# Kernel optimization log

Measured on AMD Instinct MI355X. Metric: run time of the kernel, lower is better.

## Reference

```python
import jax, jax.numpy as jnp
import numpy as np

B = 64
N_TEXT, N_VIS, N_AC = 256, 32, 32
N = N_TEXT + N_VIS + N_AC  # 320 total graph nodes
HID, HEADS, LAYERS = 512, 8, 2
HEAD_DIM = HID // HEADS
SW_K, SW_P, SF_M, ALPHA, CROSS_P = 6, 0.15, 3, 0.5, 0.3


def build_hybrid_adj():
    """Watts-Strogatz + Barabasi-Albert hybrid adjacency with cross-modal edges (numpy, setup only)."""
    rng = np.random.default_rng(0)
    # small-world ring lattice
    sw = np.zeros((N, N), np.float32)
    idx = np.arange(N)
    for j in range(1, SW_K // 2 + 1):
        sw[idx, (idx + j) % N] = 1.0
        sw[idx, (idx - j) % N] = 1.0
    # rewiring
    for i in range(N):
        for j in range(i + 1, N):
            if sw[i, j] == 1 and rng.random() < SW_P:
                sw[i, j] = sw[j, i] = 0.0
                cand = np.where(sw[i] == 0)[0]
                cand = cand[cand != i]
                if len(cand) > 0:
                    nj = rng.choice(cand)
                    sw[i, nj] = sw[nj, i] = 1.0
    # scale-free (Barabasi-Albert)
    sf = np.zeros((N, N), np.float32)
    for i in range(SF_M + 1):
        for j in range(i + 1, SF_M + 1):
            sf[i, j] = sf[j, i] = 1.0
    deg = sf.sum(1)
    for v in range(SF_M + 1, N):
        prob = deg[:v] / deg[:v].sum()
        targets = rng.choice(v, size=min(SF_M, v), replace=False, p=prob)
        sf[v, targets] = 1.0
        sf[targets, v] = 1.0
        deg = sf.sum(1)
    adj = ((ALPHA * sw + (1.0 - ALPHA) * sf) > 0.3).astype(np.float32)
    # cross-modal edges: text<->visual, text<->acoustic (Bernoulli), visual<->acoustic temporal diagonal
    ts, te = 0, N_TEXT
    vs, ve = te, te + N_VIS
    as_, ae = ve, ve + N_AC
    cm_v = (rng.random((N_TEXT, N_VIS)) < CROSS_P).astype(np.float32)
    adj[ts:te, vs:ve] = np.maximum(adj[ts:te, vs:ve], cm_v)
    adj[vs:ve, ts:te] = adj[ts:te, vs:ve].T
    cm_a = (rng.random((N_TEXT, N_AC)) < CROSS_P).astype(np.float32)
    adj[ts:te, as_:ae] = np.maximum(adj[ts:te, as_:ae], cm_a)
    adj[as_:ae, ts:te] = adj[ts:te, as_:ae].T
    k = min(N_VIS, N_AC)
    adj[vs + np.arange(k), as_ + np.arange(k)] = 1.0
    adj[as_ + np.arange(k), vs + np.arange(k)] = 1.0
    return adj.astype(np.int32)


def setup_inputs() -> dict:
    key = jax.random.key(0)
    ks = jax.random.split(key, 12)
    s = 0.02
    return {
        "text": jax.random.normal(ks[0], (B, N_TEXT, 768), jnp.float32),
        "visual": jax.random.normal(ks[1], (B, N_VIS, 47), jnp.float32),
        "acoustic": jax.random.normal(ks[2], (B, N_AC, 74), jnp.float32),
        "adj": jnp.asarray(build_hybrid_adj()),
        "Wt": jax.random.normal(ks[3], (768, HID), jnp.float32) * s,
        "Wv": jax.random.normal(ks[4], (47, HID), jnp.float32) * s,
        "Wa": jax.random.normal(ks[5], (74, HID), jnp.float32) * s,
        "Wg": jax.random.normal(ks[6], (LAYERS, HEADS, HID, HEAD_DIM), jnp.float32) * s,
        "a_src": jax.random.normal(ks[7], (LAYERS, HEADS, HEAD_DIM), jnp.float32) * s,
        "a_dst": jax.random.normal(ks[8], (LAYERS, HEADS, HEAD_DIM), jnp.float32) * s,
        "edge_logits": jax.random.normal(ks[9], (N, N), jnp.float32) * s,
    }


def _fusion(text, visual, acoustic, adj, Wt, Wv, Wa, Wg, a_src, a_dst, edge_logits):
    # project each modality into shared hidden space and stack as graph nodes
    x = jnp.concatenate([
        jnp.einsum("btd,dh->bth", text, Wt),
        jnp.einsum("bvd,dh->bvh", visual, Wv),
        jnp.einsum("bad,dh->bah", acoustic, Wa),
    ], axis=1)  # [B, N, HID]
    mask = (adj != 0)[None, None, :, :]  # [1,1,N,N]
    for l in range(LAYERS):
        h = jnp.einsum("bnd,hdf->bhnf", x, Wg[l])          # [B,H,N,Fh]
        # a([h_i || h_j]) factorizes: e_ij = a_src.h_i + a_dst.h_j
        fi = jnp.einsum("bhnf,hf->bhn", h, a_src[l])
        fj = jnp.einsum("bhnf,hf->bhn", h, a_dst[l])
        e = jax.nn.leaky_relu(fi[:, :, :, None] + fj[:, :, None, :], 0.2)
        e = e + edge_logits[None, None, :, :]               # learnable topology bias
        e = jnp.where(mask, e, -jnp.inf)                    # adjacency-masked scores
        att = jnp.nan_to_num(jax.nn.softmax(e, axis=-1))    # fully-masked rows -> 0
        out = jnp.einsum("bhij,bhjf->bhif", att, h)         # message passing
        x = out.transpose(0, 2, 1, 3).reshape(x.shape[0], N, HID)  # concat heads
        if l < LAYERS - 1:
            x = jax.nn.elu(x)
    return x  # [B, N, HID] fused node embeddings


def reference(text, visual, acoustic, adj, Wt, Wv, Wa, Wg, a_src, a_dst, edge_logits):
    return _fusion(text, visual, acoustic, adj, Wt, Wv, Wa, Wg, a_src, a_dst, edge_logits)
```

## Files before the change

### kernel.cpp

```cpp
#include <hip/hip_runtime.h>
#include <hip/hip_bf16.h>
#include <math.h>

#define BB 64
#define NN 320
#define NT 256
#define NV 32
#define NA 32
#define HIDD 512
#define NHEAD 8
#define FD 64

typedef __attribute__((ext_vector_type(8))) short bf16x8;
typedef __attribute__((ext_vector_type(4))) float floatx4;

__device__ float me_g[NN * NN];
__device__ float fif_g[512 * NN];
__device__ float fjf_g[512 * NN];
__device__ unsigned short tihi_g[16384 * 768];
__device__ unsigned short tilo_g[16384 * 768];
__device__ unsigned short vihi_g[2048 * 64];
__device__ unsigned short vilo_g[2048 * 64];
__device__ unsigned short achi_g[2048 * 128];
__device__ unsigned short aclo_g[2048 * 128];
__device__ unsigned short xhi_g[20480 * 512];
__device__ unsigned short xlo_g[20480 * 512];
__device__ unsigned short bwhi_g[512 * 768];
__device__ unsigned short bwlo_g[512 * 768];

__device__ __forceinline__ void split1(float v, unsigned short& h, unsigned short& l) {
    unsigned u = __float_as_uint(v);
    unsigned hu = u & 0xFFFF0000u;
    float lf = v - __uint_as_float(hu);
    h = (unsigned short)(hu >> 16);
    l = (unsigned short)(__float_as_uint(lf) >> 16);
}
__device__ __forceinline__ unsigned pack2(unsigned short a, unsigned short b) {
    return (unsigned)a | ((unsigned)b << 16);
}

typedef const __attribute__((address_space(1))) unsigned int* gas1_t;
typedef __attribute__((address_space(3))) unsigned int* las3_t;
__device__ __forceinline__ void gload_lds16(const void* g, void* s) {
    __builtin_amdgcn_global_load_lds((gas1_t)(unsigned long long)g,
                                     (las3_t)(unsigned)(unsigned long long)s,
                                     16, 0, 0);
}

__global__ __launch_bounds__(256) void build_me(
    const int* __restrict__ adj, const float* __restrict__ elog)
{
    const int i4 = (blockIdx.x * 256 + threadIdx.x) * 4;
    const int4   a = *(const int4*)&adj[i4];
    const float4 e = *(const float4*)&elog[i4];
    float4 m;
    m.x = a.x ? __expf(e.x) : 0.f;
    m.y = a.y ? __expf(e.y) : 0.f;
    m.z = a.z ? __expf(e.z) : 0.f;
    m.w = a.w ? __expf(e.w) : 0.f;
    *(float4*)&me_g[i4] = m;
}

__global__ __launch_bounds__(256) void presplit_A(
    const float* __restrict__ src, int M, int K, int nk, int sel)
{
    unsigned short* dh = (sel == 0) ? tihi_g : (sel == 1) ? vihi_g : achi_g;
    unsigned short* dl = (sel == 0) ? tilo_g : (sel == 1) ? vilo_g : aclo_g;
    const unsigned t = blockIdx.x * 256 + threadIdx.x;
    const unsigned lane = t & 63, rec = t >> 6;
    const unsigned kt = rec % (unsigned)nk, g = rec / (unsigned)nk;
    const int row = g * 16 + (lane & 15);
    if (row >= M) return;
    const int k0 = kt * 32 + ((lane >> 4) << 3);
    float v[8];
    if (((K & 3) == 0) && (k0 + 8 <= K)) {
        *(float4*)&v[0] = *(const float4*)&src[(size_t)row * K + k0];
        *(float4*)&v[4] = *(const float4*)&src[(size_t)row * K + k0 + 4];
    } else {
#pragma unroll
        for (int e = 0; e < 8; e++) v[e] = (k0 + e < K) ? src[(size_t)row * K + k0 + e] : 0.f;
    }
    unsigned short h[8], l[8];
#pragma unroll
    for (int e = 0; e < 8; e++) split1(v[e], h[e], l[e]);
    const size_t o = (size_t)t * 8;
    *(uint4*)&dh[o] = make_uint4(pack2(h[0],h[1]), pack2(h[2],h[3]),
                                 pack2(h[4],h[5]), pack2(h[6],h[7]));
    *(uint4*)&dl[o] = make_uint4(pack2(l[0],l[1]), pack2(l[2],l[3]),
                                 pack2(l[4],l[5]), pack2(l[6],l[7]));
}

__global__ __launch_bounds__(64) void presplit_B(
    const float* __restrict__ W, int K, int Kp, int wg_mode)
{
    const int lane = threadIdx.x;
    const int nt = blockIdx.x, kt = blockIdx.y;
    const int col = nt * 16 + (lane & 15);
    const int k0 = kt * 32 + (lane >> 4) * 8;
    unsigned short h[8], l[8];
#pragma unroll
    for (int e = 0; e < 8; e++) {
        const int k = k0 + e;
        float v = 0.f;
        if (k < K) v = wg_mode ? W[(size_t)(col >> 6) * (512 * 64) + (size_t)k * 64 + (col & 63)]
                               : W[(size_t)k * 512 + col];
        split1(v, h[e], l[e]);
    }
    const size_t o = (((size_t)nt * (Kp >> 5) + kt) * 64 + lane) * 8;
    *(uint4*)&bwhi_g[o] = make_uint4(pack2(h[0], h[1]), pack2(h[2], h[3]),
                                     pack2(h[4], h[5]), pack2(h[6], h[7]));
    *(uint4*)&bwlo_g[o] = make_uint4(pack2(l[0], l[1]), pack2(l[2], l[3]),
                                     pack2(l[4], l[5]), pack2(l[6], l[7]));
}

#define GMFMA(AH, AL, BH, BL)                                                  \
  _Pragma("unroll") for (int s = 0; s < 4; s++)                                \
  _Pragma("unroll") for (int t = 0; t < 4; t++) {                              \
      acc[s][t] = __builtin_amdgcn_mfma_f32_16x16x32_bf16(AH[s], BH[t], acc[s][t], 0, 0, 0); \
      acc[s][t] = __builtin_amdgcn_mfma_f32_16x16x32_bf16(AH[s], BL[t], acc[s][t], 0, 0, 0); \
      acc[s][t] = __builtin_amdgcn_mfma_f32_16x16x32_bf16(AL[s], BH[t], acc[s][t], 0, 0, 0); }

__global__ __launch_bounds__(256, 3) void gemm_lds(
    unsigned short* __restrict__ Hthi, unsigned short* __restrict__ Htlo,
    const float* __restrict__ asrc, const float* __restrict__ adst,
    int nk, int a_sel, int b_mode, int rpb, int noff)
{
    __shared__ __align__(16) unsigned short stage[32 * 512];

    const unsigned short* Ahi = (a_sel == 0) ? tihi_g : (a_sel == 1) ? vihi_g
                              : (a_sel == 2) ? achi_g : xhi_g;
    const unsigned short* Alo = (a_sel == 0) ? tilo_g : (a_sel == 1) ? vilo_g
                              : (a_sel == 2) ? aclo_g : xlo_g;

    const int tid = threadIdx.x, lane = tid & 63, w = tid >> 6;
    const int rw = w >> 1, cw = w & 1;
    const int m0 = blockIdx.x * 128, n0 = blockIdx.y * 128;
    const int g0 = m0 >> 4, tg0 = n0 >> 4;

    const unsigned short* plane = (w == 0) ? Ahi : (w == 1) ? Alo
                                : (w == 2) ? bwhi_g : bwlo_g;
    const unsigned rec0 = (w < 2) ? (unsigned)g0 : (unsigned)tg0;
    const unsigned short* wsrc = plane + (size_t)rec0 * nk * 512 + lane * 8;
    unsigned short* wdst = &stage[(w * 8) * 512];

    floatx4 acc[4][4];
#pragma unroll
    for (int s = 0; s < 4; s++)
#pragma unroll
        for (int t = 0; t < 4; t++) acc[s][t] = (floatx4)0.f;

    for (int kt = 0; kt < nk; ++kt) {
        __syncthreads();
#pragma unroll
        for (int u = 0; u < 8; u++)
            gload_lds16(wsrc + ((size_t)u * nk + kt) * 512, wdst + u * 512);
        __syncthreads();

        bf16x8 a_h[4], a_l[4], b_h[4], b_l[4];
#pragma unroll
        for (int s = 0; s < 4; s++) {
            a_h[s] = *(const bf16x8*)&stage[(rw * 4 + s) * 512 + lane * 8];
            a_l[s] = *(const bf16x8*)&stage[(8 + rw * 4 + s) * 512 + lane * 8];
        }
#pragma unroll
        for (int t = 0; t < 4; t++) {
            b_h[t] = *(const bf16x8*)&stage[(16 + cw * 4 + t) * 512 + lane * 8];
            b_l[t] = *(const bf16x8*)&stage[(24 + cw * 4 + t) * 512 + lane * 8];
        }
        GMFMA(a_h, a_l, b_h, b_l);
    }

    const int fq = lane & 15, rl = lane >> 4;

    if (b_mode == 0) {
        __syncthreads();
        float (*sl)[68] = (float (*)[68])(&stage[w * 2176]);
        const int ktg0 = (n0 + cw * 64) >> 5;
#pragma unroll
        for (int s = 0; s < 4; s++) {
#pragma unroll
            for (int t = 0; t < 4; t++)
#pragma unroll
                for (int r = 0; r < 4; r++)
                    sl[rl * 4 + r][t * 16 + fq] = acc[s][t][r];
            const int grow16 = m0 + rw * 64 + s * 16;
            const int b = grow16 / rpb;
            const int rr = grow16 - b * rpb;
            const unsigned g = (unsigned)b * 20 + (unsigned)((noff + rr) >> 4);
#pragma unroll
            for (int kth = 0; kth < 2; kth++) {
                float f[8];
                *(float4*)&f[0] = *(const float4*)&sl[fq][kth * 32 + rl * 8];
                *(float4*)&f[4] = *(const float4*)&sl[fq][kth * 32 + rl * 8 + 4];
                unsigned short h[8], l[8];
#pragma unroll
                for (int e = 0; e < 8; e++) split1(f[e], h[e], l[e]);
                const size_t o = (((size_t)g * 16 + ktg0 + kth) * 64 + lane) * 8;
                *(uint4*)&xhi_g[o] = make_uint4(pack2(h[0],h[1]), pack2(h[2],h[3]),
                                                pack2(h[4],h[5]), pack2(h[6],h[7]));
                *(uint4*)&xlo_g[o] = make_uint4(pack2(l[0],l[1]), pack2(l[2],l[3]),
                                                pack2(l[4],l[5]), pack2(l[6],l[7]));
            }
        }
    } else {
        const int hd = (n0 + cw * 64) >> 6;
#pragma unroll
        for (int s = 0; s < 4; s++) {
            const int m_s = m0 + rw * 64 + s * 16 + rl * 4;
            const unsigned b = (unsigned)m_s / 320u;
            const int jb = m_s - b * 320;
            const int ks = jb >> 5;
            const int jg2 = (jb >> 3) & 3;
            const int eb = jb & 7;
            const size_t slabo = (size_t)b * 8 + hd;
#pragma unroll
            for (int t = 0; t < 4; t++) {
                unsigned short h0,h1,h2,h3,l0,l1,l2,l3;
                split1(acc[s][t][0],h0,l0); split1(acc[s][t][1],h1,l1);
                split1(acc[s][t][2],h2,l2); split1(acc[s][t][3],h3,l3);
                const size_t base = (((slabo * 10 + ks) * 4 + t) * 512
                                     + (size_t)(fq | (jg2 << 4)) * 8) + eb;
                *(uint2*)&Hthi[base] = make_uint2(pack2(h0,h1), pack2(h2,h3));
                *(uint2*)&Htlo[base] = make_uint2(pack2(l0,l1), pack2(l2,l3));
            }
        }
        float as4[4], ad4[4];
#pragma unroll
        for (int t = 0; t < 4; t++) {
            as4[t] = asrc[hd * 64 + t * 16 + fq];
            ad4[t] = adst[hd * 64 + t * 16 + fq];
        }
#pragma unroll
        for (int s = 0; s < 4; s++) {
            const int m_s = m0 + rw * 64 + s * 16 + rl * 4;
            const unsigned b = (unsigned)m_s / 320u;
            const int jb = m_s - b * 320;
            float4 fi4, fj4;
#pragma unroll
            for (int r = 0; r < 4; r++) {
                float fi = (acc[s][0][r]*as4[0] + acc[s][1][r]*as4[1])
                         + (acc[s][2][r]*as4[2] + acc[s][3][r]*as4[3]);
                float fj = (acc[s][0][r]*ad4[0] + acc[s][1][r]*ad4[1])
                         + (acc[s][2][r]*ad4[2] + acc[s][3][r]*ad4[3]);
#pragma unroll
                for (int d = 1; d < 16; d <<= 1) {
                    fi += __shfl_xor(fi, d);
                    fj += __shfl_xor(fj, d);
                }
                ((float*)&fi4)[r] = fi; ((float*)&fj4)[r] = fj;
            }
            if (fq == 0) {
                const size_t o = ((size_t)b * 8 + hd) * NN + jb;
                *(float4*)&fif_g[o] = fi4;
                *(float4*)&fjf_g[o] = fj4;
            }
        }
    }
}

template<int IP0, int NIP>
__device__ __forceinline__ void attn_body(
    const unsigned short* __restrict__ Hthi, const unsigned short* __restrict__ Htlo,
    float* __restrict__ xout, int final_out, float* fjs, float* ls,
    float (*slabA)[16][68])
{
    const int bh = blockIdx.x;
    const int hd = bh & 7, b = bh >> 3;
    const int tid = threadIdx.x, lane = tid & 63, w = tid >> 6;
    const int fq = lane & 15, jg = lane >> 4;

    for (int r = tid; r < NN; r += 256) fjs[r] = fjf_g[bh * NN + r];

    float fir[NIP];
#pragma unroll
    for (int ip = 0; ip < NIP; ip++)
        fir[ip] = fif_g[bh * NN + (IP0 + ip) * 64 + (w << 4) + fq];
    __syncthreads();

    floatx4 acc[NIP][4];
#pragma unroll
    for (int ip = 0; ip < NIP; ip++)
#pragma unroll
        for (int nt = 0; nt < 4; nt++) acc[ip][nt] = (floatx4)0.f;
    float lacc[NIP];
#pragma unroll
    for (int ip = 0; ip < NIP; ip++) lacc[ip] = 0.f;

    for (int ks = 0; ks < 10; ks++) {
        const int j8 = ks * 32 + jg * 8;
        const float4 fj0 = *(const float4*)&fjs[j8];
        const float4 fj1 = *(const float4*)&fjs[j8 + 4];

        bf16x8 ahh[NIP], all[NIP];
#pragma unroll
        for (int ip = 0; ip < NIP; ip++) {
            const int i = (IP0 + ip) * 64 + (w << 4) + fq;
            const float fiv = fir[ip];
            const unsigned g = (unsigned)i * NN + j8;
            const float4 m0 = *(const float4*)&me_g[g];
            const float4 m1 = *(const float4*)&me_g[g + 4];
            float p[8];
            {
                float s;
                s = fiv + fj0.x; s = fmaxf(s, 0.2f*s); p[0] = __expf(s) * m0.x;
                s = fiv + fj0.y; s = fmaxf(s, 0.2f*s); p[1] = __expf(s) * m0.y;
                s = fiv + fj0.z; s = fmaxf(s, 0.2f*s); p[2] = __expf(s) * m0.z;
                s = fiv + fj0.w; s = fmaxf(s, 0.2f*s); p[3] = __expf(s) * m0.w;
                s = fiv + fj1.x; s = fmaxf(s, 0.2f*s); p[4] = __expf(s) * m1.x;
                s = fiv + fj1.y; s = fmaxf(s, 0.2f*s); p[5] = __expf(s) * m1.y;
                s = fiv + fj1.z; s = fmaxf(s, 0.2f*s); p[6] = __expf(s) * m1.z;
                s = fiv + fj1.w; s = fmaxf(s, 0.2f*s); p[7] = __expf(s) * m1.w;
            }
            lacc[ip] += ((p[0]+p[1]) + (p[2]+p[3])) + ((p[4]+p[5]) + (p[6]+p[7]));

            unsigned short ph[8], pl[8];
#pragma unroll
            for (int e = 0; e < 8; e++) split1(p[e], ph[e], pl[e]);
            union { uint4 u; bf16x8 v; } ua, ul;
            ua.u = make_uint4(pack2(ph[0],ph[1]), pack2(ph[2],ph[3]),
                              pack2(ph[4],ph[5]), pack2(ph[6],ph[7]));
            ul.u = make_uint4(pack2(pl[0],pl[1]), pack2(pl[2],pl[3]),
                              pack2(pl[4],pl[5]), pack2(pl[6],pl[7]));
            ahh[ip] = ua.v; all[ip] = ul.v;
        }

#pragma unroll
        for (int nt = 0; nt < 4; nt++) {
            const unsigned off = (((unsigned)bh * 10 + ks) * 4 + nt) * 512 + (unsigned)lane * 8;
            const bf16x8 bhf = *(const bf16x8*)&Hthi[off];
            const bf16x8 blf = *(const bf16x8*)&Htlo[off];
#pragma unroll
            for (int ip = 0; ip < NIP; ip++) {
                acc[ip][nt] = __builtin_amdgcn_mfma_f32_16x16x32_bf16(ahh[ip], bhf, acc[ip][nt], 0, 0, 0);
                acc[ip][nt] = __builtin_amdgcn_mfma_f32_16x16x32_bf16(ahh[ip], blf, acc[ip][nt], 0, 0, 0);
                acc[ip][nt] = __builtin_amdgcn_mfma_f32_16x16x32_bf16(all[ip], bhf, acc[ip][nt], 0, 0, 0);
            }
        }
    }

#pragma unroll
    for (int ip = 0; ip < NIP; ip++) {
        float l = lacc[ip];
        l += __shfl_xor(l, 16);
        l += __shfl_xor(l, 32);
        if (jg == 0) ls[(IP0 + ip) * 64 + (w << 4) + fq] = l;
    }
    __syncthreads();

    if (final_out) {
#pragma unroll
        for (int ip = 0; ip < NIP; ip++) {
            const int ib = ((IP0 + ip) * 4 + w) * 16 + jg * 4;
#pragma unroll
            for (int r = 0; r < 4; r++) {
                const float lv = ls[ib + r];
                const float inv = (lv > 0.f) ? 1.f / lv : 0.f;
                const size_t ro = ((size_t)(b * NN + ib + r)) * HIDD + hd * 64;
#pragma unroll
                for (int nt = 0; nt < 4; nt++)
                    xout[ro + nt * 16 + fq] = acc[ip][nt][r] * inv;
            }
        }
    } else {
        float (*sl)[68] = slabA[w];
        const int ktg0 = hd * 2;
#pragma unroll
        for (int ip = 0; ip < NIP; ip++) {
            const int ib = ((IP0 + ip) * 4 + w) * 16 + jg * 4;
#pragma unroll
            for (int r = 0; r < 4; r++) {
                const float lv = ls[ib + r];
                const float inv = (lv > 0.f) ? 1.f / lv : 0.f;
#pragma unroll
                for (int nt = 0; nt < 4; nt++) {
                    float vv = acc[ip][nt][r] * inv;
                    vv = (vv > 0.f) ? vv : __expf(vv) - 1.f;
                    sl[jg * 4 + r][nt * 16 + fq] = vv;
                }
            }
            const unsigned g = (unsigned)b * 20 + (IP0 + ip) * 4 + w;
#pragma unroll
            for (int kth = 0; kth < 2; kth++) {
                float f[8];
                *(float4*)&f[0] = *(const float4*)&sl[fq][kth * 32 + jg * 8];
                *(float4*)&f[4] = *(const float4*)&sl[fq][kth * 32 + jg * 8 + 4];
                unsigned short h[8], l[8];
#pragma unroll
                for (int e = 0; e < 8; e++) split1(f[e], h[e], l[e]);
                const size_t o = (((size_t)g * 16 + ktg0 + kth) * 64 + lane) * 8;
                *(uint4*)&xhi_g[o] = make_uint4(pack2(h[0],h[1]), pack2(h[2],h[3]),
                                                pack2(h[4],h[5]), pack2(h[6],h[7]));
                *(uint4*)&xlo_g[o] = make_uint4(pack2(l[0],l[1]), pack2(l[2],l[3]),
                                                pack2(l[4],l[5]), pack2(l[6],l[7]));
            }
        }
    }
}

__global__ __launch_bounds__(256, 4) void attn_mfma(
    const unsigned short* __restrict__ Hthi, const unsigned short* __restrict__ Htlo,
    float* __restrict__ xout, int final_out)
{
    __shared__ float fjs[NN];
    __shared__ float ls[NN];
    __shared__ float slabA[4][16][68];
    if (blockIdx.y == 0) attn_body<0, 3>(Hthi, Htlo, xout, final_out, fjs, ls, slabA);
    else                 attn_body<3, 2>(Hthi, Htlo, xout, final_out, fjs, ls, slabA);
}

extern "C" void kernel_launch(void* const* d_in, const int* in_sizes, int n_in,
                              void* d_out, int out_size, void* d_ws, size_t ws_size,
                              hipStream_t stream)
{
    (void)in_sizes; (void)n_in; (void)out_size; (void)ws_size;
    const float* text     = (const float*)d_in[0];
    const float* visual   = (const float*)d_in[1];
    const float* acoustic = (const float*)d_in[2];
    const int*   adj      = (const int*)d_in[3];
    const float* Wt       = (const float*)d_in[4];
    const float* Wv       = (const float*)d_in[5];
    const float* Wa       = (const float*)d_in[6];
    const float* Wg       = (const float*)d_in[7];
    const float* a_src    = (const float*)d_in[8];
    const float* a_dst    = (const float*)d_in[9];
    const float* elog     = (const float*)d_in[10];

    float* xbuf = (float*)d_out;
    unsigned short* Hthi = (unsigned short*)d_ws;
    unsigned short* Htlo = Hthi + (size_t)512 * 10 * 4 * 512;

    build_me<<<NN * NN / 1024, 256, 0, stream>>>(adj, elog);

    presplit_A<<<(16384 / 16) * 24 * 64 / 256, 256, 0, stream>>>(text,     16384, 768, 24, 0);
    presplit_A<<<(2048  / 16) * 2  * 64 / 256, 256, 0, stream>>>(visual,   2048,  47,  2,  1);
    presplit_A<<<(2048  / 16) * 4  * 64 / 256, 256, 0, stream>>>(acoustic, 2048,  74,  4,  2);

    presplit_B<<<dim3(32, 768 / 32), 64, 0, stream>>>(Wt, 768, 768, 0);
    gemm_lds<<<dim3((BB*NT)/128, 4), 256, 0, stream>>>(nullptr, nullptr, nullptr, nullptr,
                                                       24, 0, 0, NT, 0);
    presplit_B<<<dim3(32, 64 / 32), 64, 0, stream>>>(Wv, 47, 64, 0);
    gemm_lds<<<dim3((BB*NV)/128, 4), 256, 0, stream>>>(nullptr, nullptr, nullptr, nullptr,
                                                       2, 1, 0, NV, NT);
    presplit_B<<<dim3(32, 128 / 32), 64, 0, stream>>>(Wa, 74, 128, 0);
    gemm_lds<<<dim3((BB*NA)/128, 4), 256, 0, stream>>>(nullptr, nullptr, nullptr, nullptr,
                                                       4, 2, 0, NA, NT + NV);

    for (int l = 0; l < 2; l++) {
        const float* Wg_l = Wg + (size_t)l * NHEAD * HIDD * FD;
        presplit_B<<<dim3(32, 512 / 32), 64, 0, stream>>>(Wg_l, 512, 512, 1);
        gemm_lds<<<dim3((BB*NN)/128, 4), 256, 0, stream>>>(Hthi, Htlo,
            a_src + l * NHEAD * FD, a_dst + l * NHEAD * FD, 16, 3, 1, NN, 0);
        attn_mfma<<<dim3(BB * NHEAD, 2), 256, 0, stream>>>(
            Hthi, Htlo, xbuf, (l == 0) ? 0 : 1);
    }
}
```

Before: 364.5 us.

## Double-buffer GEMM LDS staging and prefetch attention B fragments before exp

The projection GEMM now stages its tiles in two LDS buffers. It issues the global-to-LDS loads for the next k-tile before computing on the current one, which removes one barrier per iteration and overlaps loads with MFMA. The attention kernel hoists the H^T fragment loads to the top of each k-step so their latency hides behind the exp/softmax math, and it raises wave priority around the MFMA burst. The cost is twice the LDS footprint and lower occupancy, since launch bounds drop from 3 to 2 blocks per CU.

```diff
diff --git a/kernel.cpp b/kernel.cpp
--- a/kernel.cpp
+++ b/kernel.cpp
@@ -120,12 +120,12 @@
       acc[s][t] = __builtin_amdgcn_mfma_f32_16x16x32_bf16(AH[s], BL[t], acc[s][t], 0, 0, 0); \
       acc[s][t] = __builtin_amdgcn_mfma_f32_16x16x32_bf16(AL[s], BH[t], acc[s][t], 0, 0, 0); }
 
-__global__ __launch_bounds__(256, 3) void gemm_lds(
+__global__ __launch_bounds__(256, 2) void gemm_lds(
     unsigned short* __restrict__ Hthi, unsigned short* __restrict__ Htlo,
     const float* __restrict__ asrc, const float* __restrict__ adst,
     int nk, int a_sel, int b_mode, int rpb, int noff)
 {
-    __shared__ __align__(16) unsigned short stage[32 * 512];
+    __shared__ __align__(16) unsigned short stage[2][32 * 512];
 
     const unsigned short* Ahi = (a_sel == 0) ? tihi_g : (a_sel == 1) ? vihi_g
                               : (a_sel == 2) ? achi_g : xhi_g;
@@ -141,7 +141,7 @@
                                 : (w == 2) ? bwhi_g : bwlo_g;
     const unsigned rec0 = (w < 2) ? (unsigned)g0 : (unsigned)tg0;
     const unsigned short* wsrc = plane + (size_t)rec0 * nk * 512 + lane * 8;
-    unsigned short* wdst = &stage[(w * 8) * 512];
+    const int woff = (w * 8) * 512;
 
     floatx4 acc[4][4];
 #pragma unroll
@@ -149,32 +149,40 @@
 #pragma unroll
         for (int t = 0; t < 4; t++) acc[s][t] = (floatx4)0.f;
 
+#pragma unroll
+    for (int u = 0; u < 8; u++)
+        gload_lds16(wsrc + ((size_t)u * nk) * 512, &stage[0][woff + u * 512]);
+    __syncthreads();
+
+    int cur = 0;
     for (int kt = 0; kt < nk; ++kt) {
+        if (kt + 1 < nk) {
+            unsigned short* nb = &stage[cur ^ 1][woff];
+#pragma unroll
+            for (int u = 0; u < 8; u++)
+                gload_lds16(wsrc + ((size_t)u * nk + kt + 1) * 512, nb + u * 512);
+        }
+        const unsigned short* sb = &stage[cur][0];
+        bf16x8 a_h[4], a_l[4], b_h[4], b_l[4];
+#pragma unroll
+        for (int s = 0; s < 4; s++) {
+            a_h[s] = *(const bf16x8*)&sb[(rw * 4 + s) * 512 + lane * 8];
+            a_l[s] = *(const bf16x8*)&sb[(8 + rw * 4 + s) * 512 + lane * 8];
+        }
+#pragma unroll
+        for (int t = 0; t < 4; t++) {
+            b_h[t] = *(const bf16x8*)&sb[(16 + cw * 4 + t) * 512 + lane * 8];
+            b_l[t] = *(const bf16x8*)&sb[(24 + cw * 4 + t) * 512 + lane * 8];
+        }
+        GMFMA(a_h, a_l, b_h, b_l);
         __syncthreads();
-#pragma unroll
-        for (int u = 0; u < 8; u++)
-            gload_lds16(wsrc + ((size_t)u * nk + kt) * 512, wdst + u * 512);
-        __syncthreads();
-
-        bf16x8 a_h[4], a_l[4], b_h[4], b_l[4];
-#pragma unroll
-        for (int s = 0; s < 4; s++) {
-            a_h[s] = *(const bf16x8*)&stage[(rw * 4 + s) * 512 + lane * 8];
-            a_l[s] = *(const bf16x8*)&stage[(8 + rw * 4 + s) * 512 + lane * 8];
-        }
-#pragma unroll
-        for (int t = 0; t < 4; t++) {
-            b_h[t] = *(const bf16x8*)&stage[(16 + cw * 4 + t) * 512 + lane * 8];
-            b_l[t] = *(const bf16x8*)&stage[(24 + cw * 4 + t) * 512 + lane * 8];
-        }
-        GMFMA(a_h, a_l, b_h, b_l);
+        cur ^= 1;
     }
 
     const int fq = lane & 15, rl = lane >> 4;
 
     if (b_mode == 0) {
-        __syncthreads();
-        float (*sl)[68] = (float (*)[68])(&stage[w * 2176]);
+        float (*sl)[68] = (float (*)[68])(&stage[0][w * 2176]);
         const int ktg0 = (n0 + cw * 64) >> 5;
 #pragma unroll
         for (int s = 0; s < 4; s++) {
@@ -287,6 +295,14 @@
     for (int ip = 0; ip < NIP; ip++) lacc[ip] = 0.f;
 
     for (int ks = 0; ks < 10; ks++) {
+        bf16x8 bhf[4], blf[4];
+#pragma unroll
+        for (int nt = 0; nt < 4; nt++) {
+            const unsigned off = (((unsigned)bh * 10 + ks) * 4 + nt) * 512 + (unsigned)lane * 8;
+            bhf[nt] = *(const bf16x8*)&Hthi[off];
+            blf[nt] = *(const bf16x8*)&Htlo[off];
+        }
+
         const int j8 = ks * 32 + jg * 8;
         const float4 fj0 = *(const float4*)&fjs[j8];
         const float4 fj1 = *(const float4*)&fjs[j8 + 4];
@@ -324,18 +340,16 @@
             ahh[ip] = ua.v; all[ip] = ul.v;
         }
 
-#pragma unroll
-        for (int nt = 0; nt < 4; nt++) {
-            const unsigned off = (((unsigned)bh * 10 + ks) * 4 + nt) * 512 + (unsigned)lane * 8;
-            const bf16x8 bhf = *(const bf16x8*)&Hthi[off];
-            const bf16x8 blf = *(const bf16x8*)&Htlo[off];
+        __builtin_amdgcn_s_setprio(1);
+#pragma unroll
+        for (int nt = 0; nt < 4; nt++)
 #pragma unroll
             for (int ip = 0; ip < NIP; ip++) {
-                acc[ip][nt] = __builtin_amdgcn_mfma_f32_16x16x32_bf16(ahh[ip], bhf, acc[ip][nt], 0, 0, 0);
-                acc[ip][nt] = __builtin_amdgcn_mfma_f32_16x16x32_bf16(ahh[ip], blf, acc[ip][nt], 0, 0, 0);
-                acc[ip][nt] = __builtin_amdgcn_mfma_f32_16x16x32_bf16(all[ip], bhf, acc[ip][nt], 0, 0, 0);
-            }
-        }
+                acc[ip][nt] = __builtin_amdgcn_mfma_f32_16x16x32_bf16(ahh[ip], bhf[nt], acc[ip][nt], 0, 0, 0);
+                acc[ip][nt] = __builtin_amdgcn_mfma_f32_16x16x32_bf16(ahh[ip], blf[nt], acc[ip][nt], 0, 0, 0);
+                acc[ip][nt] = __builtin_amdgcn_mfma_f32_16x16x32_bf16(all[ip], bhf[nt], acc[ip][nt], 0, 0, 0);
+            }
+        __builtin_amdgcn_s_setprio(0);
     }
 
 #pragma unroll
```

Result: slower. 406.1 us (+11.4%).
